# Kernel tuning notes

Measured on AMD Instinct MI355X. Metric: run time of the kernel, lower is better.

Reference implementation:

```python
import jax, jax.numpy as jnp
import numpy as np

ALPHA = 0.2  # leaky relu negative slope


def setup_inputs() -> dict:
    key = jax.random.key(0)
    k1, k2, k3, k4 = jax.random.split(key, 4)
    B, N, F_in, F_out = 8, 2048, 128, 64
    node_input = jax.random.normal(k1, (B, N, F_in), dtype=jnp.float32)
    adj = jax.random.randint(k2, (B, N, N), 0, 2, dtype=jnp.int32)
    node_mask = jnp.ones((B, N), dtype=jnp.float32)
    W = jax.random.normal(k3, (F_in, F_out), dtype=jnp.float32) * (1.414 * (6.0 / (F_in + F_out)) ** 0.5 / 1.7)
    a = jax.random.normal(k4, (2 * F_out, 1), dtype=jnp.float32) * 0.1
    return {"node_input": node_input, "adj": adj, "node_mask": node_mask, "W": W, "a": a}


def reference(node_input, adj, node_mask, W, a):
    d = W.shape[1]
    h = jnp.matmul(node_input, W)                      # [B, N, d]
    # score[b,i,j] = leakyrelu(h_i . a[:d] + h_j . a[d:]) -- decomposed pairwise concat
    e_src = jnp.matmul(h, a[:d, 0])                    # [B, N]
    e_dst = jnp.matmul(h, a[d:, 0])                    # [B, N]
    score = jax.nn.leaky_relu(e_src[:, :, None] + e_dst[:, None, :], negative_slope=ALPHA)
    scores = jnp.where(adj == 1, score, jnp.zeros((), score.dtype))
    attention = jnp.where(adj > 0, scores, jnp.full((), -30.0, score.dtype))
    h = h * node_mask[:, :, None]
    attn = jax.nn.softmax(attention, axis=2)           # softmax over j
    # h_prime[b,j] = sum_i attn[b,i,j] * h[b,i]  (sum over dim=1, as in the torch code)
    h_prime = jnp.einsum('bij,bid->bjd', attn, h)
    return jax.nn.elu(h_prime)
```

## Files before the change

### kernel.cpp

```cpp
#include <hip/hip_runtime.h>
#include <stdint.h>

typedef unsigned int uint32;
typedef unsigned long long u64;
typedef short bf16x8 __attribute__((ext_vector_type(8)));
typedef float f32x4 __attribute__((ext_vector_type(4)));

__device__ __forceinline__ unsigned short f2bf(float f) {
  uint32 u = __builtin_bit_cast(uint32, f);
  u += 0x7FFFu + ((u >> 16) & 1u);
  return (unsigned short)(u >> 16);
}

__global__ __launch_bounds__(256) void k1_h_e(
    const float* __restrict__ X, const float* __restrict__ W,
    const float* __restrict__ A, const float* __restrict__ mask,
    unsigned short* __restrict__ hTt,
    float* __restrict__ E1, float* __restrict__ E2,
    float* __restrict__ ET, float* __restrict__ G) {
  __shared__ float WT[64][132];
  const int t = threadIdx.x;
  for (int idx = t; idx < 128 * 64; idx += 256) {
    int k = idx >> 6, d = idx & 63;
    WT[d][k] = W[idx];
  }
  __syncthreads();

  const int dg = t & 15;
  const int rp = t >> 4;
  const int gi0 = blockIdx.x * 32 + rp * 2;

  float a1[4], a2[4];
#pragma unroll
  for (int dd = 0; dd < 4; ++dd) {
    a1[dd] = A[dg + 16 * dd];
    a2[dd] = A[64 + dg + 16 * dd];
  }

  const float4* x0 = (const float4*)(X + (size_t)gi0 * 128);
  const float4* x1 = (const float4*)(X + (size_t)(gi0 + 1) * 128);
  float h0[4] = {0.f, 0.f, 0.f, 0.f}, h1[4] = {0.f, 0.f, 0.f, 0.f};
#pragma unroll 4
  for (int kq = 0; kq < 32; ++kq) {
    const float4 xa = x0[kq], xb = x1[kq];
#pragma unroll
    for (int dd = 0; dd < 4; ++dd) {
      const float4 w4 = *(const float4*)(&WT[dg + 16 * dd][kq * 4]);
      h0[dd] += xa.x * w4.x + xa.y * w4.y + xa.z * w4.z + xa.w * w4.w;
      h1[dd] += xb.x * w4.x + xb.y * w4.y + xb.z * w4.z + xb.w * w4.w;
    }
  }

  float es0 = 0.f, ed0 = 0.f, es1 = 0.f, ed1 = 0.f;
#pragma unroll
  for (int dd = 0; dd < 4; ++dd) {
    es0 += h0[dd] * a1[dd]; ed0 += h0[dd] * a2[dd];
    es1 += h1[dd] * a1[dd]; ed1 += h1[dd] * a2[dd];
  }
#pragma unroll
  for (int m = 1; m < 16; m <<= 1) {
    es0 += __shfl_xor(es0, m, 64);
    ed0 += __shfl_xor(ed0, m, 64);
    es1 += __shfl_xor(es1, m, 64);
    ed1 += __shfl_xor(ed1, m, 64);
  }
  if (dg == 0) {
    ET[gi0] = expf(-es0);      G[gi0] = expf(0.8f * es0);
    E1[gi0] = expf(ed0);       E2[gi0] = expf(0.2f * ed0);
    ET[gi0 + 1] = expf(-es1);  G[gi0 + 1] = expf(0.8f * es1);
    E1[gi0 + 1] = expf(ed1);   E2[gi0 + 1] = expf(0.2f * ed1);
  }

  const float m0 = mask[gi0], m1 = mask[gi0 + 1];
  const int b = gi0 >> 11, i = gi0 & 2047;
  const int ib = i >> 3, io = i & 7;
#pragma unroll
  for (int dd = 0; dd < 4; ++dd) {
    const int d = dg + 16 * dd;
    const uint32 lo = f2bf(h0[dd] * m0);
    const uint32 hi = f2bf(h1[dd] * m1);
    *(uint32*)(hTt + ((size_t)b << 17) + (ib << 9) + (d << 3) + io) = lo | (hi << 16);
  }
}

__global__ __launch_bounds__(256) void k3_stats(
    const int* __restrict__ adj,
    const float* __restrict__ E1, const float* __restrict__ E2,
    const float* __restrict__ ET, const float* __restrict__ G,
    uint32* __restrict__ bitA, uint32* __restrict__ bitB,
    uint32* __restrict__ PP) {
  const int w = threadIdx.x >> 6, lane = threadIdx.x & 63;
  const int gi = blockIdx.x * 4 + w;
  const int b = gi >> 11, i = gi & 2047;
  const float eti = ET[gi];
  const int4* arow = (const int4*)(adj + (size_t)gi * 2048);
  const float4* e1p = (const float4*)(E1 + b * 2048);
  const float4* e2p = (const float4*)(E2 + b * 2048);
  float s1 = 0.f, s2 = 0.f;
#pragma unroll
  for (int jc = 0; jc < 8; ++jc) {
    const int idx = jc * 64 + lane;
    const int4 av = arow[idx];
    const float4 e1 = e1p[idx];
    const float4 e2 = e2p[idx];
    const bool m0 = (av.x == 1), m1b = (av.y == 1), m2 = (av.z == 1), m3 = (av.w == 1);
    const bool q0 = (e1.x > eti), q1 = (e1.y > eti), q2 = (e1.z > eti), q3 = (e1.w > eti);
    s1 += (m0 && q0) ? e1.x : 0.f;   s2 += (m0 && !q0) ? e2.x : 0.f;
    s1 += (m1b && q1) ? e1.y : 0.f;  s2 += (m1b && !q1) ? e2.y : 0.f;
    s1 += (m2 && q2) ? e1.z : 0.f;   s2 += (m2 && !q2) ? e2.z : 0.f;
    s1 += (m3 && q3) ? e1.w : 0.f;   s2 += (m3 && !q3) ? e2.w : 0.f;
    const u64 b0 = __ballot(m0), b1 = __ballot(m1b), b2 = __ballot(m2), b3 = __ballot(m3);
    if (lane < 4) {
      const u64 v = (lane == 0) ? b0 : (lane == 1) ? b1 : (lane == 2) ? b2 : b3;
      const size_t off = (size_t)(b * 32 + jc * 4 + lane) * 2048 + i;
      bitA[off] = (uint32)v;
      bitB[off] = (uint32)(v >> 32);
    }
  }
#pragma unroll
  for (int m = 1; m < 64; m <<= 1) {
    s1 += __shfl_xor(s1, m, 64);
    s2 += __shfl_xor(s2, m, 64);
  }
  if (lane == 0) {
    const float g = G[gi];
    const bool ok = (s1 + s2) > 0.f;
    const float p1 = ok ? 1.f / (s1 + s2 / g) : 0.f;
    const float p2 = ok ? 1.f / (s1 * g + s2) : 0.f;
    PP[gi] = (uint32)f2bf(p1) | ((uint32)f2bf(p2) << 16);
  }
}

__global__ __launch_bounds__(256) void k4_fused(
    const unsigned short* __restrict__ hTt,
    const uint32* __restrict__ bitA, const uint32* __restrict__ bitB,
    const float* __restrict__ E1, const float* __restrict__ E2,
    const uint32* __restrict__ PP, float* __restrict__ out) {
  __shared__ float sAcc[3][16][68];
  const int t = threadIdx.x;
  const int w = t >> 6, l = t & 63;
  const int bid = blockIdx.x;
  const int b = bid & 7;
  const int jt = bid >> 3;
  const int J0 = jt * 16;
  const int jj = J0 + (l & 15);
  const int kg = l >> 4;

  const float rE1 = E1[b * 2048 + jj];
  const float rE2 = E2[b * 2048 + jj];
  const int widx = ((jj >> 8) << 2) + (jj & 3);
  const size_t rowoff = (size_t)(b * 32 + widx) * 2048;
  const int sh = (jj >> 2) & 63;
  const uint32 maskbit = 1u << (sh & 31);
  const uint32* bp = ((sh >= 32) ? bitB : bitA) + rowoff;
  const uint32* PPb = PP + b * 2048;
  const unsigned short* hTtb = hTt + ((size_t)b << 17);

  f32x4 acc[4] = {};

  const int ib0 = w * 512 + kg * 8;
  uint4 bq0 = *(const uint4*)(bp + ib0);
  uint4 bq1 = *(const uint4*)(bp + ib0 + 4);
  uint4 pq0 = *(const uint4*)(PPb + ib0);
  uint4 pq1 = *(const uint4*)(PPb + ib0 + 4);

#pragma unroll
  for (int kt = 0; kt < 16; ++kt) {
    const int i0 = w * 512 + kt * 32;

    const size_t bbase = ((size_t)((i0 >> 3) + kg)) << 9;
    const bf16x8 bv0 = *(const bf16x8*)(hTtb + bbase + (((l & 15) + 0) << 3));
    const bf16x8 bv1 = *(const bf16x8*)(hTtb + bbase + (((l & 15) + 16) << 3));
    const bf16x8 bv2 = *(const bf16x8*)(hTtb + bbase + (((l & 15) + 32) << 3));
    const bf16x8 bv3 = *(const bf16x8*)(hTtb + bbase + (((l & 15) + 48) << 3));

    uint4 nbq0 = bq0, nbq1 = bq1, npq0 = pq0, npq1 = pq1;
    if (kt < 15) {
      const int ni = i0 + 32 + kg * 8;
      nbq0 = *(const uint4*)(bp + ni);
      nbq1 = *(const uint4*)(bp + ni + 4);
      npq0 = *(const uint4*)(PPb + ni);
      npq1 = *(const uint4*)(PPb + ni + 4);
    }

    auto pv = [&](uint32 dw, uint32 pp) -> uint32 {
      const float p1f = __builtin_bit_cast(float, pp << 16);
      const float p2f = __builtin_bit_cast(float, pp & 0xFFFF0000u);
      const float v = fmaxf(p1f * rE1, p2f * rE2);
      return (dw & maskbit) ? __builtin_bit_cast(uint32, v) : 0u;
    };
    uint32 pe[8];
    pe[0] = pv(bq0.x, pq0.x);
    pe[1] = pv(bq0.y, pq0.y);
    pe[2] = pv(bq0.z, pq0.z);
    pe[3] = pv(bq0.w, pq0.w);
    pe[4] = pv(bq1.x, pq1.x);
    pe[5] = pv(bq1.y, pq1.y);
    pe[6] = pv(bq1.z, pq1.z);
    pe[7] = pv(bq1.w, pq1.w);

    union { uint32 u4[4]; bf16x8 v; } af;
#pragma unroll
    for (int e = 0; e < 4; ++e)
      af.u4[e] = (pe[2 * e + 1] & 0xFFFF0000u) | (pe[2 * e] >> 16);

    acc[0] = __builtin_amdgcn_mfma_f32_16x16x32_bf16(af.v, bv0, acc[0], 0, 0, 0);
    acc[1] = __builtin_amdgcn_mfma_f32_16x16x32_bf16(af.v, bv1, acc[1], 0, 0, 0);
    acc[2] = __builtin_amdgcn_mfma_f32_16x16x32_bf16(af.v, bv2, acc[2], 0, 0, 0);
    acc[3] = __builtin_amdgcn_mfma_f32_16x16x32_bf16(af.v, bv3, acc[3], 0, 0, 0);

    bq0 = nbq0; bq1 = nbq1; pq0 = npq0; pq1 = npq1;
  }

  if (w > 0) {
#pragma unroll
    for (int dt = 0; dt < 4; ++dt)
#pragma unroll
      for (int r = 0; r < 4; ++r)
        sAcc[w - 1][(l >> 4) * 4 + r][dt * 16 + (l & 15)] = acc[dt][r];
  }
  __syncthreads();
  if (w == 0) {
    float* outb = out + ((size_t)b << 17);
#pragma unroll
    for (int dt = 0; dt < 4; ++dt) {
#pragma unroll
      for (int r = 0; r < 4; ++r) {
        const int jrow = (l >> 4) * 4 + r;
        const int d = dt * 16 + (l & 15);
        float s = acc[dt][r] + sAcc[0][jrow][d] + sAcc[1][jrow][d] + sAcc[2][jrow][d];
        s = s > 0.f ? s : expm1f(s);
        outb[(size_t)(J0 + jrow) * 64 + d] = s;
      }
    }
  }
}

extern "C" void kernel_launch(void* const* d_in, const int* in_sizes, int n_in,
                              void* d_out, int out_size, void* d_ws, size_t ws_size,
                              hipStream_t stream) {
  const float* X = (const float*)d_in[0];
  const int* adj = (const int*)d_in[1];
  const float* mask = (const float*)d_in[2];
  const float* W = (const float*)d_in[3];
  const float* A = (const float*)d_in[4];
  float* out = (float*)d_out;
  char* ws = (char*)d_ws;

  unsigned short* hTt = (unsigned short*)(ws);
  float* E1 = (float*)(ws + 2097152);
  float* E2 = (float*)(ws + 2162688);
  float* ET = (float*)(ws + 2228224);
  float* G  = (float*)(ws + 2293760);
  uint32* PP = (uint32*)(ws + 2359296);
  uint32* bitA = (uint32*)(ws + 2424832);
  uint32* bitB = (uint32*)(ws + 4521984);

  hipLaunchKernelGGL(k1_h_e, dim3(512), dim3(256), 0, stream, X, W, A, mask, hTt, E1, E2, ET, G);
  hipLaunchKernelGGL(k3_stats, dim3(4096), dim3(256), 0, stream, adj, E1, E2, ET, G, bitA, bitB, PP);
  hipLaunchKernelGGL(k4_fused, dim3(1024), dim3(256), 0, stream, hTt, bitA, bitB, E1, E2, PP, out);
}
```

Baseline: 74.48 us.

## Double-buffer h tiles in LDS via async global_load_lds in fused kernel

The fused attention-aggregation kernel now streams each wave's 32-row slice of transposed h into a per-wave double-buffered LDS tile using direct global-to-LDS loads, prefetching the next slice while the current one feeds the MFMAs. Previously each lane fetched the B operand straight from global memory every iteration. Each iteration now begins with a full vmcnt(0) wait, which also serialises the bitmask/PP prefetches. The last iteration issues a redundant wrap-around load, and the extra 32KB of LDS may reduce occupancy.

```diff
diff --git a/kernel.cpp b/kernel.cpp
--- a/kernel.cpp
+++ b/kernel.cpp
@@ -10,6 +10,12 @@
   uint32 u = __builtin_bit_cast(uint32, f);
   u += 0x7FFFu + ((u >> 16) & 1u);
   return (unsigned short)(u >> 16);
+}
+
+__device__ __forceinline__ void gload_lds16(const void* g, void* l) {
+  __builtin_amdgcn_global_load_lds(
+      (const __attribute__((address_space(1))) void*)g,
+      (__attribute__((address_space(3))) void*)l, 16, 0, 0);
 }
 
 __global__ __launch_bounds__(256) void k1_h_e(
@@ -136,6 +142,7 @@
     const uint32* __restrict__ bitA, const uint32* __restrict__ bitB,
     const float* __restrict__ E1, const float* __restrict__ E2,
     const uint32* __restrict__ PP, float* __restrict__ out) {
+  __shared__ unsigned short tile[4][2][2048];
   __shared__ float sAcc[3][16][68];
   const int t = threadIdx.x;
   const int w = t >> 6, l = t & 63;
@@ -154,10 +161,17 @@
   const uint32 maskbit = 1u << (sh & 31);
   const uint32* bp = ((sh >= 32) ? bitB : bitA) + rowoff;
   const uint32* PPb = PP + b * 2048;
-  const unsigned short* hTtb = hTt + ((size_t)b << 17);
+  const char* hTtB = (const char*)(hTt + ((size_t)b << 17));
 
   f32x4 acc[4] = {};
 
+  {
+    const char* gs = hTtB + (((size_t)(w * 512 >> 3)) << 10) + (l << 4);
+    gload_lds16(gs, &tile[w][0][0]);
+    gload_lds16(gs + 1024, &tile[w][0][512]);
+    gload_lds16(gs + 2048, &tile[w][0][1024]);
+    gload_lds16(gs + 3072, &tile[w][0][1536]);
+  }
   const int ib0 = w * 512 + kg * 8;
   uint4 bq0 = *(const uint4*)(bp + ib0);
   uint4 bq1 = *(const uint4*)(bp + ib0 + 4);
@@ -166,22 +180,23 @@
 
 #pragma unroll
   for (int kt = 0; kt < 16; ++kt) {
-    const int i0 = w * 512 + kt * 32;
-
-    const size_t bbase = ((size_t)((i0 >> 3) + kg)) << 9;
-    const bf16x8 bv0 = *(const bf16x8*)(hTtb + bbase + (((l & 15) + 0) << 3));
-    const bf16x8 bv1 = *(const bf16x8*)(hTtb + bbase + (((l & 15) + 16) << 3));
-    const bf16x8 bv2 = *(const bf16x8*)(hTtb + bbase + (((l & 15) + 32) << 3));
-    const bf16x8 bv3 = *(const bf16x8*)(hTtb + bbase + (((l & 15) + 48) << 3));
-
-    uint4 nbq0 = bq0, nbq1 = bq1, npq0 = pq0, npq1 = pq1;
-    if (kt < 15) {
-      const int ni = i0 + 32 + kg * 8;
-      nbq0 = *(const uint4*)(bp + ni);
-      nbq1 = *(const uint4*)(bp + ni + 4);
-      npq0 = *(const uint4*)(PPb + ni);
-      npq1 = *(const uint4*)(PPb + ni + 4);
-    }
+    asm volatile("s_waitcnt vmcnt(0)" ::: "memory");
+    __builtin_amdgcn_sched_barrier(0);
+
+    const int i0n = w * 512 + ((kt + 1) & 15) * 32;
+    {
+      const char* gs = hTtB + (((size_t)(i0n >> 3)) << 10) + (l << 4);
+      unsigned short* ld = &tile[w][(kt + 1) & 1][0];
+      gload_lds16(gs, ld);
+      gload_lds16(gs + 1024, ld + 512);
+      gload_lds16(gs + 2048, ld + 1024);
+      gload_lds16(gs + 3072, ld + 1536);
+    }
+    const int ni = i0n + kg * 8;
+    const uint4 nbq0 = *(const uint4*)(bp + ni);
+    const uint4 nbq1 = *(const uint4*)(bp + ni + 4);
+    const uint4 npq0 = *(const uint4*)(PPb + ni);
+    const uint4 npq1 = *(const uint4*)(PPb + ni + 4);
 
     auto pv = [&](uint32 dw, uint32 pp) -> uint32 {
       const float p1f = __builtin_bit_cast(float, pp << 16);
@@ -204,6 +219,12 @@
     for (int e = 0; e < 4; ++e)
       af.u4[e] = (pe[2 * e + 1] & 0xFFFF0000u) | (pe[2 * e] >> 16);
 
+    const unsigned short* tl = &tile[w][kt & 1][kg * 512];
+    const bf16x8 bv0 = *(const bf16x8*)(tl + (((l & 15) + 0) << 3));
+    const bf16x8 bv1 = *(const bf16x8*)(tl + (((l & 15) + 16) << 3));
+    const bf16x8 bv2 = *(const bf16x8*)(tl + (((l & 15) + 32) << 3));
+    const bf16x8 bv3 = *(const bf16x8*)(tl + (((l & 15) + 48) << 3));
+
     acc[0] = __builtin_amdgcn_mfma_f32_16x16x32_bf16(af.v, bv0, acc[0], 0, 0, 0);
     acc[1] = __builtin_amdgcn_mfma_f32_16x16x32_bf16(af.v, bv1, acc[1], 0, 0, 0);
     acc[2] = __builtin_amdgcn_mfma_f32_16x16x32_bf16(af.v, bv2, acc[2], 0, 0, 0);
```

After: 86.18 us. +15.7%, slower.

## Stage adjacency bit rows and PP in LDS, prefetch hTt operands

Applied to the files above, without the earlier changes.

The fused aggregation kernel now cooperatively loads the four adjacency bit-rows used by its 16-column tile, plus the per-batch PP array, into LDS up front, instead of each lane issuing strided global loads per iteration. The software prefetch moves from the bit/PP data to the bf16 h operand tiles for the next k step. LDS is reused for the cross-wave reduction. This cuts redundant global traffic but adds a block-wide barrier and around 41KB of LDS, which may lower occupancy.

```diff
diff --git a/kernel.cpp b/kernel.cpp
--- a/kernel.cpp
+++ b/kernel.cpp
@@ -136,7 +136,11 @@
     const uint32* __restrict__ bitA, const uint32* __restrict__ bitB,
     const float* __restrict__ E1, const float* __restrict__ E2,
     const uint32* __restrict__ PP, float* __restrict__ out) {
-  __shared__ float sAcc[3][16][68];
+  __shared__ __align__(16) char raw[41024];
+  uint32* bitsL = (uint32*)raw;
+  uint32* ppL = (uint32*)(raw + 32832);
+  float* sa = (float*)raw;
+
   const int t = threadIdx.x;
   const int w = t >> 6, l = t & 63;
   const int bid = blockIdx.x;
@@ -148,40 +152,47 @@
 
   const float rE1 = E1[b * 2048 + jj];
   const float rE2 = E2[b * 2048 + jj];
-  const int widx = ((jj >> 8) << 2) + (jj & 3);
-  const size_t rowoff = (size_t)(b * 32 + widx) * 2048;
+  const int widxBase = (J0 >> 8) << 2;
   const int sh = (jj >> 2) & 63;
   const uint32 maskbit = 1u << (sh & 31);
-  const uint32* bp = ((sh >= 32) ? bitB : bitA) + rowoff;
+  const uint32* plane = (sh >= 32) ? bitB : bitA;
+  const uint32* rowBase = plane + (size_t)(b * 32 + widxBase) * 2048;
   const uint32* PPb = PP + b * 2048;
   const unsigned short* hTtb = hTt + ((size_t)b << 17);
 
+  for (int idx = t; idx < 2048; idx += 256) {
+    const int r = idx >> 9, c = (idx & 511) << 2;
+    *(uint4*)&bitsL[r * 2052 + c] = *(const uint4*)(rowBase + (size_t)r * 2048 + c);
+  }
+  for (int idx = t; idx < 512; idx += 256)
+    *(uint4*)&ppL[idx << 2] = *(const uint4*)(PPb + (idx << 2));
+  __syncthreads();
+
   f32x4 acc[4] = {};
-
-  const int ib0 = w * 512 + kg * 8;
-  uint4 bq0 = *(const uint4*)(bp + ib0);
-  uint4 bq1 = *(const uint4*)(bp + ib0 + 4);
-  uint4 pq0 = *(const uint4*)(PPb + ib0);
-  uint4 pq1 = *(const uint4*)(PPb + ib0 + 4);
+  const int arow = (l & 3) * 2052;
+  const int lane15_3 = (l & 15) << 3;
+
+  size_t bb = ((size_t)((w * 512) >> 3) + kg) << 9;
+  bf16x8 bv0 = *(const bf16x8*)(hTtb + bb + lane15_3);
+  bf16x8 bv1 = *(const bf16x8*)(hTtb + bb + lane15_3 + 128);
+  bf16x8 bv2 = *(const bf16x8*)(hTtb + bb + lane15_3 + 256);
+  bf16x8 bv3 = *(const bf16x8*)(hTtb + bb + lane15_3 + 384);
 
 #pragma unroll
   for (int kt = 0; kt < 16; ++kt) {
-    const int i0 = w * 512 + kt * 32;
-
-    const size_t bbase = ((size_t)((i0 >> 3) + kg)) << 9;
-    const bf16x8 bv0 = *(const bf16x8*)(hTtb + bbase + (((l & 15) + 0) << 3));
-    const bf16x8 bv1 = *(const bf16x8*)(hTtb + bbase + (((l & 15) + 16) << 3));
-    const bf16x8 bv2 = *(const bf16x8*)(hTtb + bbase + (((l & 15) + 32) << 3));
-    const bf16x8 bv3 = *(const bf16x8*)(hTtb + bbase + (((l & 15) + 48) << 3));
-
-    uint4 nbq0 = bq0, nbq1 = bq1, npq0 = pq0, npq1 = pq1;
-    if (kt < 15) {
-      const int ni = i0 + 32 + kg * 8;
-      nbq0 = *(const uint4*)(bp + ni);
-      nbq1 = *(const uint4*)(bp + ni + 4);
-      npq0 = *(const uint4*)(PPb + ni);
-      npq1 = *(const uint4*)(PPb + ni + 4);
-    }
+    const int ibi = w * 512 + kt * 32 + kg * 8;
+
+    const uint4 bq0 = *(const uint4*)&bitsL[arow + ibi];
+    const uint4 bq1 = *(const uint4*)&bitsL[arow + ibi + 4];
+    const uint4 pq0 = *(const uint4*)&ppL[ibi];
+    const uint4 pq1 = *(const uint4*)&ppL[ibi + 4];
+
+    const int i0n = w * 512 + ((kt + 1) & 15) * 32;
+    const size_t nbb = ((size_t)(i0n >> 3) + kg) << 9;
+    const bf16x8 nv0 = *(const bf16x8*)(hTtb + nbb + lane15_3);
+    const bf16x8 nv1 = *(const bf16x8*)(hTtb + nbb + lane15_3 + 128);
+    const bf16x8 nv2 = *(const bf16x8*)(hTtb + nbb + lane15_3 + 256);
+    const bf16x8 nv3 = *(const bf16x8*)(hTtb + nbb + lane15_3 + 384);
 
     auto pv = [&](uint32 dw, uint32 pp) -> uint32 {
       const float p1f = __builtin_bit_cast(float, pp << 16);
@@ -209,15 +220,16 @@
     acc[2] = __builtin_amdgcn_mfma_f32_16x16x32_bf16(af.v, bv2, acc[2], 0, 0, 0);
     acc[3] = __builtin_amdgcn_mfma_f32_16x16x32_bf16(af.v, bv3, acc[3], 0, 0, 0);
 
-    bq0 = nbq0; bq1 = nbq1; pq0 = npq0; pq1 = npq1;
-  }
-
+    bv0 = nv0; bv1 = nv1; bv2 = nv2; bv3 = nv3;
+  }
+
+  __syncthreads();
   if (w > 0) {
 #pragma unroll
     for (int dt = 0; dt < 4; ++dt)
 #pragma unroll
       for (int r = 0; r < 4; ++r)
-        sAcc[w - 1][(l >> 4) * 4 + r][dt * 16 + (l & 15)] = acc[dt][r];
+        sa[(w - 1) * 1088 + ((l >> 4) * 4 + r) * 68 + dt * 16 + (l & 15)] = acc[dt][r];
   }
   __syncthreads();
   if (w == 0) {
@@ -228,7 +240,8 @@
       for (int r = 0; r < 4; ++r) {
         const int jrow = (l >> 4) * 4 + r;
         const int d = dt * 16 + (l & 15);
-        float s = acc[dt][r] + sAcc[0][jrow][d] + sAcc[1][jrow][d] + sAcc[2][jrow][d];
+        float s = acc[dt][r] + sa[jrow * 68 + d] + sa[1088 + jrow * 68 + d] +
+                  sa[2176 + jrow * 68 + d];
         s = s > 0.f ? s : expm1f(s);
         outb[(size_t)(J0 + jrow) * 64 + d] = s;
       }
```

New measurement: 67.58 us. 9.3% less time.
